# Optimization experiments

Measured on AMD Instinct MI355X. Metric: run time of the kernel, lower is better.

The kernel has to match this reference:

```python
import jax, jax.numpy as jnp
import numpy as np

LMAX = 4
NCOEF = (LMAX + 1) ** 2  # 25 spherical-harmonic coefficients
EXPAND = np.repeat(np.arange(LMAX + 1), [2 * l + 1 for l in range(LMAX + 1)])  # per-l -> per-(l,m)
N, E, C, H, HEADS, ACH, VCH, F, G, DE, AEMB, MAXEL = 10000, 50000, 64, 64, 8, 16, 8, 128, 36, 32, 32, 100


def setup_inputs() -> dict:
    ks = jax.random.split(jax.random.key(0), 24)
    f = lambda i, shape, s=1.0: jax.random.normal(ks[i], shape, jnp.float32) * s
    return dict(
        x=f(0, (N, NCOEF, C)),
        edge_index=jax.random.randint(ks[1], (2, E), 0, N),
        atomic_numbers=jax.random.randint(ks[2], (N,), 0, MAXEL),
        edge_distance=jax.random.uniform(ks[3], (E, DE), jnp.float32),
        wigner=f(4, (E, NCOEF, NCOEF), 0.2),
        src_tab=f(5, (MAXEL, AEMB), 0.02), tgt_tab=f(6, (MAXEL, AEMB), 0.02),
        rad_w1=f(7, (DE + 2 * AEMB, 64), 0.1), rad_b1=jnp.zeros((64,), jnp.float32),
        rad_w2=f(8, (64, 64), 0.1), rad_b2=jnp.zeros((64,), jnp.float32),
        rad_w3=f(9, (64, (LMAX + 1) * 2 * C), 0.05), rad_b3=jnp.ones(((LMAX + 1) * 2 * C,), jnp.float32),
        W1=f(10, (2 * C, H), 0.05), W0_extra=f(11, (2 * C, HEADS * ACH + H), 0.05),
        alpha_dot=f(12, (HEADS, ACH), 0.1),
        to_grid=f(13, (G, NCOEF), 0.2), from_grid=f(14, (NCOEF, G), 0.2),
        proj_out=f(15, (HEADS * VCH, C), 0.1),
        gamma1=jnp.ones((C,), jnp.float32), gamma2=jnp.ones((C,), jnp.float32),
        gl_w=f(16, (C, F), 0.1), gl_b=jnp.zeros((F,), jnp.float32),
        ffn_w1=f(17, (C, F), 0.1), ffn_b1=jnp.zeros((F,), jnp.float32),
        ffn_w2=f(18, (F, C), 0.1), ffn_b2=jnp.zeros((C,), jnp.float32),
    )


def _rmsnorm(x, gamma, eps=1e-6):
    # equivariant norm over the coefficient axis, per node/channel
    rms = jnp.sqrt(jnp.mean(x * x, axis=1, keepdims=True) + eps)  # [N,1,C]
    return x / rms * gamma


def _s2_sep_act(gate, x, to_grid, from_grid):
    # separable S2 activation: scalars = silu(gating scalars); l>0 via grid SiLU
    grid = jnp.einsum('gi,nih->ngh', to_grid, x)
    xg = jnp.einsum('ig,ngh->nih', from_grid, jax.nn.silu(grid))
    return jnp.concatenate([jax.nn.silu(gate)[:, None, :], xg[:, 1:, :]], axis=1)


def reference(x, edge_index, atomic_numbers, edge_distance, wigner, src_tab, tgt_tab,
              rad_w1, rad_b1, rad_w2, rad_b2, rad_w3, rad_b3,
              W1, W0_extra, alpha_dot, to_grid, from_grid, proj_out,
              gamma1, gamma2, gl_w, gl_b, ffn_w1, ffn_b1, ffn_w2, ffn_b2):
    src, dst = edge_index[0], edge_index[1]
    # ---- SO2 equivariant graph attention (gather -> rotate -> conv -> act -> attn -> scatter) ----
    h = _rmsnorm(x, gamma1)
    xe = jnp.concatenate([h[src], h[dst]], axis=-1)          # [E,25,2C] edge gather
    xe = jnp.einsum('eij,ejc->eic', wigner, xe)              # rotate into edge frame
    ef = jnp.concatenate([edge_distance, src_tab[atomic_numbers[src]],
                          tgt_tab[atomic_numbers[dst]]], axis=-1)
    r = jax.nn.silu(ef @ rad_w1 + rad_b1)
    r = jax.nn.silu(r @ rad_w2 + rad_b2)
    r = (r @ rad_w3 + rad_b3).reshape(-1, LMAX + 1, 2 * C)[:, EXPAND, :]  # m-shared radial, [E,25,2C]
    xe = xe * r
    extra = xe[:, 0, :] @ W0_extra                           # extra m=0 channels
    alpha_f = extra[:, :HEADS * ACH].reshape(-1, HEADS, ACH)
    gate = extra[:, HEADS * ACH:]                            # [E,H]
    msg = jnp.einsum('eic,ch->eih', xe, W1)                  # [E,25,H]
    msg = _s2_sep_act(gate, msg, to_grid, from_grid)
    # attention weights: softmax over incoming edges of each destination node
    alpha = jnp.einsum('eha,ha->eh', jax.nn.silu(alpha_f), alpha_dot)
    amax = jax.lax.stop_gradient(jax.ops.segment_max(alpha, dst, num_segments=N))
    a = jnp.exp(alpha - amax[dst])
    a = a / (jax.ops.segment_sum(a, dst, num_segments=N)[dst] + 1e-8)
    msg = (msg.reshape(-1, NCOEF, HEADS, VCH) * a[:, None, :, None]).reshape(-1, NCOEF, HEADS * VCH)
    msg = jnp.einsum('eji,ejc->eic', wigner, msg)            # rotate back (D^T)
    agg = jax.ops.segment_sum(msg, dst, num_segments=N)      # scatter-add, [N,25,H]
    x = x + agg @ proj_out
    # ---- feed-forward with separable S2 activation ----
    h = _rmsnorm(x, gamma2)
    gate = h[:, 0, :] @ gl_w + gl_b
    f1 = jnp.einsum('nic,cf->nif', h, ffn_w1)
    f1 = jnp.concatenate([f1[:, :1, :] + ffn_b1, f1[:, 1:, :]], axis=1)  # bias on l=0 only
    f1 = _s2_sep_act(gate, f1, to_grid, from_grid)
    f2 = jnp.einsum('nif,fc->nic', f1, ffn_w2)
    f2 = jnp.concatenate([f2[:, :1, :] + ffn_b2, f2[:, 1:, :]], axis=1)
    return x + f2
```

## Files before the change

kernel.cpp:

```cpp
#include <hip/hip_runtime.h>
#include <hip/hip_bf16.h>

#define NN 10000
#define NE 50000

typedef __attribute__((ext_vector_type(8))) short bfrag8;
typedef __attribute__((ext_vector_type(4))) short s16x4;
typedef __attribute__((ext_vector_type(4))) float f32x4;

__device__ __forceinline__ float silu_f(float v){ return v / (1.0f + __expf(-v)); }
__device__ __forceinline__ short f2b(float f){
  unsigned u = __float_as_uint(f);
  u += 0x7fffu + ((u>>16)&1u);
  return (short)(u>>16);
}
__device__ __forceinline__ float b2f(short s){
  return __uint_as_float(((unsigned)(unsigned short)s)<<16);
}

__global__ __launch_bounds__(256) void k_rms1(const float* __restrict__ x,
                                              const float* __restrict__ gamma,
                                              __hip_bfloat16* __restrict__ h){
  int idx = blockIdx.x*256 + threadIdx.x;
  if (idx >= NN*64) return;
  int n = idx>>6, c = idx&63;
  const float* xp = x + (size_t)n*1600 + c;
  float ss = 0.f;
#pragma unroll
  for (int i=0;i<25;i++){ float v = xp[i*64]; ss += v*v; }
  float inv = gamma[c] * rsqrtf(ss*(1.f/25.f) + 1e-6f);
  __hip_bfloat16* hp = h + (size_t)n*1600 + c;
#pragma unroll
  for (int i=0;i<25;i++) hp[i*64] = __float2bfloat16(xp[i*64]*inv);
}

__global__ void k_wprep(const float* __restrict__ W1, const float* __restrict__ tog,
                        const float* __restrict__ fromg, const float* __restrict__ proj,
                        const float* __restrict__ fw1, const float* __restrict__ fw2,
                        const float* __restrict__ rw1, const float* __restrict__ rw2,
                        const float* __restrict__ rw3, const float* __restrict__ w0e,
                        short* __restrict__ w1t, short* __restrict__ togA,
                        short* __restrict__ fgA, short* __restrict__ projT,
                        short* __restrict__ fw1T, short* __restrict__ fw2T,
                        short* __restrict__ rw1T, short* __restrict__ rw2T,
                        short* __restrict__ rw3T, short* __restrict__ w0eP){
  int t0 = blockIdx.x*blockDim.x + threadIdx.x;
  int stride = gridDim.x*blockDim.x;
  for (int idx=t0; idx<64*136; idx+=stride){
    int hh = idx/136, k = idx-136*hh;
    w1t[idx] = (k<128) ? f2b(W1[k*64+hh]) : (short)0;
  }
  for (int idx=t0; idx<48*40; idx+=stride){
    int g = idx/40, i = idx-40*g;
    togA[idx] = (g<36 && i<25) ? f2b(tog[g*25+i]) : (short)0;
  }
  for (int idx=t0; idx<32*72; idx+=stride){
    int j = idx/72, g = idx-72*j;
    fgA[idx] = (j<25 && g<36) ? f2b(fromg[j*36+g]) : (short)0;
  }
  for (int idx=t0; idx<64*64; idx+=stride){
    int c = idx>>6, k = idx&63;
    projT[idx] = f2b(proj[k*64+c]);
  }
  for (int idx=t0; idx<128*64; idx+=stride){
    int f = idx>>6, c = idx&63;
    fw1T[idx] = f2b(fw1[c*128+f]);
  }
  for (int idx=t0; idx<64*128; idx+=stride){
    int c = idx>>7, f = idx&127;
    fw2T[idx] = f2b(fw2[f*64+c]);
  }
  for (int idx=t0; idx<64*96; idx+=stride){
    int n = idx/96, k = idx-96*n;
    rw1T[idx] = f2b(rw1[k*64+n]);
  }
  for (int idx=t0; idx<64*64; idx+=stride){
    int n = idx>>6, k = idx&63;
    rw2T[idx] = f2b(rw2[k*64+n]);
  }
  for (int idx=t0; idx<640*64; idx+=stride){
    int n = idx>>6, k = idx&63;
    rw3T[idx] = f2b(rw3[(size_t)k*640+n]);
  }
  for (int idx=t0; idx<128*192; idx+=stride)
    w0eP[idx] = f2b(w0e[idx]);
}

__global__ __launch_bounds__(256,4) void k_radial(
  const int* __restrict__ ei, const int* __restrict__ an,
  const float* __restrict__ edist,
  const float* __restrict__ stab, const float* __restrict__ ttab,
  const short* __restrict__ rw1T, const float* __restrict__ rb1,
  const short* __restrict__ rw2T, const float* __restrict__ rb2,
  const short* __restrict__ rw3T, const float* __restrict__ rb3,
  short* __restrict__ rfS)
{
  __shared__ __align__(16) short SP[7936];
  const int tid = threadIdx.x;
  const int wv = tid>>6, lane = tid&63, lo = lane&15, q = lane>>4;
  const int e0 = blockIdx.x*32;
  {
    int e = tid>>3;
    int ee = min(e0+e, NE-1);
    int srcE = ei[ee], dstE = ei[NE+ee];
    const float* dp = edist + (size_t)ee*32;
    const float* sp = stab + (size_t)an[srcE]*32;
    const float* tp = ttab + (size_t)an[dstE]*32;
    int kb = tid&7;
#pragma unroll
    for (int it=0; it<12; ++it){
      int k = kb + it*8;
      float v = (k<32) ? dp[k] : (k<64 ? sp[k-32] : tp[k-64]);
      SP[e*104+k] = f2b(v);
    }
  }
  __syncthreads();
  {
    f32x4 zf={0.f,0.f,0.f,0.f}; f32x4 acc[2]={zf,zf};
#pragma unroll
    for (int kt=0;kt<3;kt++){
      bfrag8 a = *(const bfrag8*)&rw1T[(wv*16+lo)*96 + kt*32 + q*8];
#pragma unroll
      for (int et=0;et<2;et++){
        bfrag8 b = *(const bfrag8*)&SP[(et*16+lo)*104 + kt*32 + q*8];
        acc[et] = __builtin_amdgcn_mfma_f32_16x16x32_bf16(a,b,acc[et],0,0,0);
      }
    }
    int n1 = wv*16 + q*4;
    const float4 bb = *(const float4*)&rb1[n1];
#pragma unroll
    for (int et=0;et<2;et++){
      s16x4 o;
      o[0]=f2b(silu_f(acc[et][0]+bb.x)); o[1]=f2b(silu_f(acc[et][1]+bb.y));
      o[2]=f2b(silu_f(acc[et][2]+bb.z)); o[3]=f2b(silu_f(acc[et][3]+bb.w));
      *(s16x4*)&SP[3328 + (et*16+lo)*72 + n1] = o;
    }
  }
  __syncthreads();
  {
    f32x4 zf={0.f,0.f,0.f,0.f}; f32x4 acc[2]={zf,zf};
#pragma unroll
    for (int kt=0;kt<2;kt++){
      bfrag8 a = *(const bfrag8*)&rw2T[(wv*16+lo)*64 + kt*32 + q*8];
#pragma unroll
      for (int et=0;et<2;et++){
        bfrag8 b = *(const bfrag8*)&SP[3328 + (et*16+lo)*72 + kt*32 + q*8];
        acc[et] = __builtin_amdgcn_mfma_f32_16x16x32_bf16(a,b,acc[et],0,0,0);
      }
    }
    int n2 = wv*16 + q*4;
    const float4 bb = *(const float4*)&rb2[n2];
#pragma unroll
    for (int et=0;et<2;et++){
      s16x4 o;
      o[0]=f2b(silu_f(acc[et][0]+bb.x)); o[1]=f2b(silu_f(acc[et][1]+bb.y));
      o[2]=f2b(silu_f(acc[et][2]+bb.z)); o[3]=f2b(silu_f(acc[et][3]+bb.w));
      *(s16x4*)&SP[5632 + (et*16+lo)*72 + n2] = o;
    }
  }
  __syncthreads();
  {
    bfrag8 bfr[2][2];
#pragma unroll
    for (int et=0;et<2;et++)
#pragma unroll
      for (int kt=0;kt<2;kt++)
        bfr[et][kt] = *(const bfrag8*)&SP[5632 + (et*16+lo)*72 + kt*32 + q*8];
    for (int mi=0; mi<10; ++mi){
      int n3base = (wv + mi*4)*16;
      f32x4 zf={0.f,0.f,0.f,0.f}; f32x4 acc[2]={zf,zf};
#pragma unroll
      for (int kt=0;kt<2;kt++){
        bfrag8 a = *(const bfrag8*)&rw3T[(size_t)(n3base+lo)*64 + kt*32 + q*8];
        acc[0] = __builtin_amdgcn_mfma_f32_16x16x32_bf16(a,bfr[0][kt],acc[0],0,0,0);
        acc[1] = __builtin_amdgcn_mfma_f32_16x16x32_bf16(a,bfr[1][kt],acc[1],0,0,0);
      }
      int n3 = n3base + q*4;
      const float4 bb = *(const float4*)&rb3[n3];
#pragma unroll
      for (int et=0;et<2;et++){
        int e = e0 + et*16 + lo;
        if (e < NE){
          s16x4 o;
          o[0]=f2b(acc[et][0]+bb.x); o[1]=f2b(acc[et][1]+bb.y);
          o[2]=f2b(acc[et][2]+bb.z); o[3]=f2b(acc[et][3]+bb.w);
          *(s16x4*)&rfS[(size_t)e*640 + n3] = o;
        }
      }
    }
  }
}

__global__ __launch_bounds__(256,4) void k_edge(
  const __hip_bfloat16* __restrict__ h, const int* __restrict__ ei,
  const float* __restrict__ wig,
  const short* __restrict__ w1t, const short* __restrict__ togA,
  const short* __restrict__ fgA, const short* __restrict__ w0eP,
  const float* __restrict__ adot,
  const short* __restrict__ rfS, float* __restrict__ asum,
  float* __restrict__ agg)
{
  __shared__ __align__(16) short POOL[16288];
  float* rfull = (float*)&POOL[14592];
  float* gateL = (float*)&POOL[15872];
  float* ahead = (float*)&POOL[16000];
  float* exL   = (float*)&POOL[16032];
  const int tid = threadIdx.x;
  const int wv = tid>>6, lane = tid&63, lo = lane&15, q = lane>>4;
  const int e = blockIdx.x;
  const int src = ei[e], dst = ei[NE+e];

  {
    int4 z; z.x=0; z.y=0; z.z=0; z.w=0;
    int4* zp = (int4*)POOL;
    for (int idx=tid; idx<960; idx+=256) zp[idx] = z;
  }
  __syncthreads();
  for (int idx=tid; idx<625; idx+=256){
    int i = idx/25, j = idx-25*i;
    short v = f2b(wig[(size_t)e*625+idx]);
    POOL[5120 + i*40 + j] = v;
    POOL[6400 + j*40 + i] = v;
  }
  {
    const __hip_bfloat16* hs = h + (size_t)src*1600;
    const __hip_bfloat16* hd = h + (size_t)dst*1600;
    for (int idx=tid; idx<400; idx+=256){
      int nh = idx/200, rem = idx-200*nh;
      int j = rem>>3, cg = rem&7;
      const __hip_bfloat16* hp = nh ? hd : hs;
      uint4 v = *(const uint4*)(hp + j*64 + cg*8);
      unsigned el[8] = {v.x&0xffffu, v.x>>16, v.y&0xffffu, v.y>>16,
                        v.z&0xffffu, v.z>>16, v.w&0xffffu, v.w>>16};
      int cb = nh*64 + cg*8;
#pragma unroll
      for (int qq=0;qq<8;qq++) POOL[(cb+qq)*40 + j] = (short)el[qq];
    }
  }
  for (int idx=tid; idx<640; idx+=256) rfull[idx] = b2f(rfS[(size_t)e*640+idx]);
  __syncthreads();

  {
    f32x4 zf = {0.f,0.f,0.f,0.f};
    f32x4 acc[2][2] = {{zf,zf},{zf,zf}};
    bfrag8 b0 = *(const bfrag8*)&POOL[5120 + (lo)*40 + q*8];
    bfrag8 b1 = *(const bfrag8*)&POOL[5120 + (16+lo)*40 + q*8];
#pragma unroll
    for (int t=0;t<2;t++){
      int mrow = (2*wv+t)*16 + lo;
      bfrag8 a = *(const bfrag8*)&POOL[mrow*40 + q*8];
      acc[t][0] = __builtin_amdgcn_mfma_f32_16x16x32_bf16(a, b0, acc[t][0], 0,0,0);
      acc[t][1] = __builtin_amdgcn_mfma_f32_16x16x32_bf16(a, b1, acc[t][1], 0,0,0);
    }
#pragma unroll
    for (int t=0;t<2;t++){
      int c0 = (2*wv+t)*16 + q*4;
#pragma unroll
      for (int nt=0;nt<2;nt++){
        int i = nt*16 + lo;
        int l = (i>=16)?4:((i>=9)?3:((i>=4)?2:((i>=1)?1:0)));
        const f32x4 rv = *(const f32x4*)&rfull[l*128 + c0];
        s16x4 o;
#pragma unroll
        for (int r=0;r<4;r++) o[r] = f2b(acc[t][nt][r]*rv[r]);
        *(s16x4*)&POOL[7680 + i*136 + c0] = o;
      }
    }
  }
  __syncthreads();

  {
    if (tid < 96){
      float s0=0.f, s1=0.f;
      for (int c=0; c<128; c+=2){
        unsigned xp = *(const unsigned*)&POOL[7680 + c];
        float x0 = b2f((short)(xp&0xffffu)), x1 = b2f((short)(xp>>16));
        unsigned wp0 = *(const unsigned*)&w0eP[c*192 + 2*tid];
        unsigned wp1 = *(const unsigned*)&w0eP[(c+1)*192 + 2*tid];
        s0 += x0*b2f((short)(wp0&0xffffu)) + x1*b2f((short)(wp1&0xffffu));
        s1 += x0*b2f((short)(wp0>>16))     + x1*b2f((short)(wp1>>16));
      }
      if (tid < 64){
        int n0 = 2*tid;
        exL[n0]   = silu_f(s0)*adot[n0];
        exL[n0+1] = silu_f(s1)*adot[n0+1];
      } else {
        int g0 = 2*tid - 128;
        gateL[g0]   = silu_f(s0);
        gateL[g0+1] = silu_f(s1);
      }
    }
  }
  {
    const int hh = wv*16 + lo;
    f32x4 zf = {0.f,0.f,0.f,0.f};
    f32x4 acc[2] = {zf,zf};
#pragma unroll
    for (int kt=0;kt<4;kt++){
      bfrag8 b = *(const bfrag8*)&w1t[hh*136 + kt*32 + q*8];
#pragma unroll
      for (int t=0;t<2;t++){
        bfrag8 a = *(const bfrag8*)&POOL[7680 + (t*16+lo)*136 + kt*32 + q*8];
        acc[t] = __builtin_amdgcn_mfma_f32_16x16x32_bf16(a, b, acc[t], 0,0,0);
      }
    }
#pragma unroll
    for (int t=0;t<2;t++){
      s16x4 o;
#pragma unroll
      for (int r=0;r<4;r++) o[r] = f2b(acc[t][r]);
      *(s16x4*)&POOL[12032 + hh*40 + t*16 + q*4] = o;
    }
  }
  __syncthreads();

  if (tid < 8){
    float s = 0.f;
#pragma unroll
    for (int a=0;a<16;a++) s += exL[tid*16+a];
    float eh = __expf(s);
    ahead[tid] = eh;
    unsafeAtomicAdd(&asum[(size_t)dst*8 + tid], eh);
  }
  {
    const int hh = wv*16 + lo;
    bfrag8 b = *(const bfrag8*)&POOL[12032 + hh*40 + q*8];
    f32x4 zf = {0.f,0.f,0.f,0.f};
    f32x4 acc[3] = {zf,zf,zf};
#pragma unroll
    for (int t=0;t<3;t++){
      bfrag8 a = *(const bfrag8*)&togA[(t*16+lo)*40 + q*8];
      acc[t] = __builtin_amdgcn_mfma_f32_16x16x32_bf16(a, b, acc[t], 0,0,0);
    }
#pragma unroll
    for (int t=0;t<3;t++){
      s16x4 o;
#pragma unroll
      for (int r=0;r<4;r++) o[r] = f2b(silu_f(acc[t][r]));
      *(s16x4*)&POOL[hh*72 + t*16 + q*4] = o;
    }
  }
  __syncthreads();

  {
    const int hh = wv*16 + lo;
    f32x4 zf = {0.f,0.f,0.f,0.f};
    f32x4 acc[2] = {zf,zf};
#pragma unroll
    for (int kt=0;kt<2;kt++){
      bfrag8 b = *(const bfrag8*)&POOL[hh*72 + kt*32 + q*8];
#pragma unroll
      for (int t=0;t<2;t++){
        bfrag8 a = *(const bfrag8*)&fgA[(t*16+lo)*72 + kt*32 + q*8];
        acc[t] = __builtin_amdgcn_mfma_f32_16x16x32_bf16(a, b, acc[t], 0,0,0);
      }
    }
    float ah = ahead[hh>>3];
#pragma unroll
    for (int t=0;t<2;t++){
      s16x4 o;
#pragma unroll
      for (int r=0;r<4;r++){
        int j = t*16 + q*4 + r;
        float v = acc[t][r];
        if (j==0) v = gateL[hh];
        o[r] = f2b(v*ah);
      }
      *(s16x4*)&POOL[7680 + hh*40 + t*16 + q*4] = o;
    }
  }
  __syncthreads();

  {
    const int hh = wv*16 + lo;
    bfrag8 b = *(const bfrag8*)&POOL[7680 + hh*40 + q*8];
    f32x4 zf = {0.f,0.f,0.f,0.f};
    f32x4 acc[2] = {zf,zf};
#pragma unroll
    for (int t=0;t<2;t++){
      bfrag8 a = *(const bfrag8*)&POOL[6400 + (t*16+lo)*40 + q*8];
      acc[t] = __builtin_amdgcn_mfma_f32_16x16x32_bf16(a, b, acc[t], 0,0,0);
    }
    float* aggp = agg + (size_t)dst*1600;
#pragma unroll
    for (int t=0;t<2;t++){
#pragma unroll
      for (int r=0;r<4;r++){
        int i = t*16 + q*4 + r;
        if (i<25) unsafeAtomicAdd(&aggp[i*64+hh], acc[t][r]);
      }
    }
  }
}

__global__ __launch_bounds__(256,4) void k_node(
  const float* __restrict__ x, const float* __restrict__ aggin,
  const float* __restrict__ asum,
  const short* __restrict__ projT, const float* __restrict__ gamma2,
  const float* __restrict__ glw, const float* __restrict__ glb,
  const short* __restrict__ fw1T, const float* __restrict__ fb1,
  const short* __restrict__ fw2T, const float* __restrict__ fb2,
  const short* __restrict__ togA, const short* __restrict__ fgA,
  float* __restrict__ out)
{
  __shared__ __align__(16) short P[19072];
  float* xF    = (float*)P;
  short* sgB   = P + 4352;
  short* hh2B  = P + 4352;
  short* f1B   = P + 13568;
  short* aggB  = P + 13568;
  short* xgB   = P + 13568;
  float* invc  = ((float*)P) + 9344;
  float* gateF = ((float*)P) + 9408;
  const int tid = threadIdx.x;
  const int wv = tid>>6, lane = tid&63, lo = lane&15, q = lane>>4;
  const int n = blockIdx.x;
  const s16x4 z4 = {0,0,0,0};

  for (int idx=tid; idx<400; idx+=256){
    int i = idx>>4, k = idx&15;
    float sc = 1.f/(asum[(size_t)n*8 + (k>>1)] + 1e-8f);
    const float4 v = *(const float4*)(aggin + (size_t)n*1600 + (size_t)idx*4);
    s16x4 o; o[0]=f2b(v.x*sc); o[1]=f2b(v.y*sc); o[2]=f2b(v.z*sc); o[3]=f2b(v.w*sc);
    *(s16x4*)&aggB[i*72 + k*4] = o;
  }
  for (int idx=tid; idx<126; idx+=256)
    *(s16x4*)&hh2B[25*72 + idx*4] = z4;
  for (int idx=tid; idx<512; idx+=256){
    int f = idx>>2, gg = 48 + (idx&3)*4;
    *(s16x4*)&sgB[f*72 + gg] = z4;
  }
  __syncthreads();

  {
    f32x4 zf={0.f,0.f,0.f,0.f}; f32x4 acc[2]={zf,zf};
    const int c = wv*16 + lo;
#pragma unroll
    for (int kt=0;kt<2;kt++){
      bfrag8 b = *(const bfrag8*)&projT[c*64 + kt*32 + q*8];
#pragma unroll
      for (int t=0;t<2;t++){
        bfrag8 a = *(const bfrag8*)&aggB[(t*16+lo)*72 + kt*32 + q*8];
        acc[t] = __builtin_amdgcn_mfma_f32_16x16x32_bf16(a,b,acc[t],0,0,0);
      }
    }
#pragma unroll
    for (int t=0;t<2;t++)
#pragma unroll
      for (int r=0;r<4;r++){
        int i = t*16 + q*4 + r;
        if (i<25) xF[i*68+c] = acc[t][r] + x[(size_t)n*1600 + i*64 + c];
      }
  }
  __syncthreads();
  if (tid<64){
    float ss=0.f;
#pragma unroll
    for (int i=0;i<25;i++){ float v = xF[i*68+tid]; ss += v*v; }
    invc[tid] = gamma2[tid]*rsqrtf(ss*(1.f/25.f)+1e-6f);
  }
  __syncthreads();
  for (int idx=tid; idx<1600; idx+=256){
    int i=idx>>6, c=idx&63;
    hh2B[i*72+c] = f2b(xF[i*68+c]*invc[c]);
  }
  if (tid<128){
    float a = glb[tid];
#pragma unroll 8
    for (int c=0;c<64;c++) a += xF[c]*invc[c]*glw[c*128+tid];
    gateF[tid] = silu_f(a);
  }
  __syncthreads();

  {
    f32x4 zf={0.f,0.f,0.f,0.f}; f32x4 acc[2][2]={{zf,zf},{zf,zf}};
#pragma unroll
    for (int kt=0;kt<2;kt++){
      bfrag8 a0 = *(const bfrag8*)&hh2B[(lo)*72 + kt*32 + q*8];
      bfrag8 a1 = *(const bfrag8*)&hh2B[(16+lo)*72 + kt*32 + q*8];
#pragma unroll
      for (int s=0;s<2;s++){
        int f = wv*32 + s*16 + lo;
        bfrag8 b = *(const bfrag8*)&fw1T[f*64 + kt*32 + q*8];
        acc[0][s] = __builtin_amdgcn_mfma_f32_16x16x32_bf16(a0,b,acc[0][s],0,0,0);
        acc[1][s] = __builtin_amdgcn_mfma_f32_16x16x32_bf16(a1,b,acc[1][s],0,0,0);
      }
    }
#pragma unroll
    for (int s=0;s<2;s++){
      int f = wv*32 + s*16 + lo;
      float bb = fb1[f];
#pragma unroll
      for (int t=0;t<2;t++){
        s16x4 o;
#pragma unroll
        for (int r=0;r<4;r++){
          int i = t*16+q*4+r;
          o[r] = f2b(acc[t][s][r] + (i==0 ? bb : 0.f));
        }
        *(s16x4*)&f1B[f*40 + t*16 + q*4] = o;
      }
    }
  }
  __syncthreads();

  {
    f32x4 zf={0.f,0.f,0.f,0.f}; f32x4 acc[3][2]={{zf,zf},{zf,zf},{zf,zf}};
    bfrag8 a0 = *(const bfrag8*)&togA[(lo)*40 + q*8];
    bfrag8 a1 = *(const bfrag8*)&togA[(16+lo)*40 + q*8];
    bfrag8 a2 = *(const bfrag8*)&togA[(32+lo)*40 + q*8];
#pragma unroll
    for (int s=0;s<2;s++){
      int f = wv*32 + s*16 + lo;
      bfrag8 b = *(const bfrag8*)&f1B[f*40 + q*8];
      acc[0][s] = __builtin_amdgcn_mfma_f32_16x16x32_bf16(a0,b,acc[0][s],0,0,0);
      acc[1][s] = __builtin_amdgcn_mfma_f32_16x16x32_bf16(a1,b,acc[1][s],0,0,0);
      acc[2][s] = __builtin_amdgcn_mfma_f32_16x16x32_bf16(a2,b,acc[2][s],0,0,0);
    }
#pragma unroll
    for (int s=0;s<2;s++){
      int f = wv*32 + s*16 + lo;
#pragma unroll
      for (int t=0;t<3;t++){
        s16x4 o;
#pragma unroll
        for (int r=0;r<4;r++) o[r] = f2b(silu_f(acc[t][s][r]));
        *(s16x4*)&sgB[f*72 + t*16 + q*4] = o;
      }
    }
  }
  __syncthreads();

  {
    f32x4 zf={0.f,0.f,0.f,0.f}; f32x4 acc[2][2]={{zf,zf},{zf,zf}};
#pragma unroll
    for (int kt=0;kt<2;kt++){
#pragma unroll
      for (int t=0;t<2;t++){
        bfrag8 b = *(const bfrag8*)&fgA[(t*16+lo)*72 + kt*32 + q*8];
#pragma unroll
        for (int s=0;s<2;s++){
          bfrag8 a = *(const bfrag8*)&sgB[(wv*32+s*16+lo)*72 + kt*32 + q*8];
          acc[s][t] = __builtin_amdgcn_mfma_f32_16x16x32_bf16(a,b,acc[s][t],0,0,0);
        }
      }
    }
#pragma unroll
    for (int s=0;s<2;s++){
      int f0 = wv*32 + s*16 + q*4;
#pragma unroll
      for (int t=0;t<2;t++){
        int j = t*16 + lo;
        s16x4 o;
#pragma unroll
        for (int r=0;r<4;r++)
          o[r] = f2b(j==0 ? gateF[f0+r] : acc[s][t][r]);
        *(s16x4*)&xgB[j*136 + f0] = o;
      }
    }
  }
  __syncthreads();

  {
    f32x4 zf={0.f,0.f,0.f,0.f}; f32x4 acc[2]={zf,zf};
    const int c = wv*16 + lo;
#pragma unroll
    for (int kt=0;kt<4;kt++){
      bfrag8 b = *(const bfrag8*)&fw2T[c*128 + kt*32 + q*8];
#pragma unroll
      for (int t=0;t<2;t++){
        bfrag8 a = *(const bfrag8*)&xgB[(t*16+lo)*136 + kt*32 + q*8];
        acc[t] = __builtin_amdgcn_mfma_f32_16x16x32_bf16(a,b,acc[t],0,0,0);
      }
    }
    float bb = fb2[c];
#pragma unroll
    for (int t=0;t<2;t++)
#pragma unroll
      for (int r=0;r<4;r++){
        int i = t*16 + q*4 + r;
        if (i<25)
          out[(size_t)n*1600 + i*64 + c] = xF[i*68+c] + acc[t][r] + (i==0 ? bb : 0.f);
      }
  }
}

extern "C" void kernel_launch(void* const* d_in, const int* in_sizes, int n_in,
                              void* d_out, int out_size, void* d_ws, size_t ws_size,
                              hipStream_t stream) {
  (void)in_sizes; (void)n_in; (void)ws_size;
  const float* x     = (const float*)d_in[0];
  const int*   ei    = (const int*)d_in[1];
  const int*   an    = (const int*)d_in[2];
  const float* edist = (const float*)d_in[3];
  const float* wig   = (const float*)d_in[4];
  const float* stab  = (const float*)d_in[5];
  const float* ttab  = (const float*)d_in[6];
  const float* rw1   = (const float*)d_in[7];
  const float* rb1   = (const float*)d_in[8];
  const float* rw2   = (const float*)d_in[9];
  const float* rb2   = (const float*)d_in[10];
  const float* rw3   = (const float*)d_in[11];
  const float* rb3   = (const float*)d_in[12];
  const float* W1    = (const float*)d_in[13];
  const float* w0e   = (const float*)d_in[14];
  const float* adot  = (const float*)d_in[15];
  const float* tog   = (const float*)d_in[16];
  const float* fromg = (const float*)d_in[17];
  const float* proj  = (const float*)d_in[18];
  const float* g1    = (const float*)d_in[19];
  const float* g2    = (const float*)d_in[20];
  const float* glw   = (const float*)d_in[21];
  const float* glb   = (const float*)d_in[22];
  const float* fw1   = (const float*)d_in[23];
  const float* fb1   = (const float*)d_in[24];
  const float* fw2   = (const float*)d_in[25];
  const float* fb2   = (const float*)d_in[26];
  float* out = (float*)d_out;

  char* wsb = (char*)d_ws;
  __hip_bfloat16* hbuf = (__hip_bfloat16*)(wsb);
  short* rfS   = (short*)(wsb + 32000000);
  float* asum  = (float*)(wsb + 96000000);
  short* w1t   = (short*)(wsb + 96320128);
  short* togA  = (short*)(wsb + 96337600);
  short* fgA   = (short*)(wsb + 96341504);
  short* projT = (short*)(wsb + 96346112);
  short* fw1T  = (short*)(wsb + 96354304);
  short* fw2T  = (short*)(wsb + 96370688);
  short* rw1T  = (short*)(wsb + 96387072);
  short* rw2T  = (short*)(wsb + 96399360);
  short* rw3T  = (short*)(wsb + 96407552);
  short* w0eP  = (short*)(wsb + 96489472);

  hipMemsetAsync(asum, 0, (size_t)NN*8*sizeof(float), stream);
  hipMemsetAsync(d_out, 0, (size_t)out_size*sizeof(float), stream);

  k_wprep<<<32, 256, 0, stream>>>(W1, tog, fromg, proj, fw1, fw2, rw1, rw2, rw3, w0e,
                                  w1t, togA, fgA, projT, fw1T, fw2T,
                                  rw1T, rw2T, rw3T, w0eP);
  k_rms1  <<<(NN*64+255)/256, 256, 0, stream>>>(x, g1, hbuf);
  k_radial<<<(NE+31)/32, 256, 0, stream>>>(ei, an, edist, stab, ttab,
                                           rw1T, rb1, rw2T, rb2, rw3T, rb3, rfS);
  k_edge  <<<NE, 256, 0, stream>>>(hbuf, ei, wig, w1t, togA, fgA, w0eP, adot,
                                   rfS, asum, out);
  k_node  <<<NN, 256, 0, stream>>>(x, out, asum, projT, g2, glw, glb,
                                   fw1T, fb1, fw2T, fb2, togA, fgA, out);
}
```

Measured before the change: 1.115 ms.

## Pre-transpose wigner and node features, async LDS loads, MFMA alpha projection in edge kernel

```diff
diff --git a/kernel.cpp b/kernel.cpp
--- a/kernel.cpp
+++ b/kernel.cpp
@@ -6,6 +6,7 @@
 
 typedef __attribute__((ext_vector_type(8))) short bfrag8;
 typedef __attribute__((ext_vector_type(4))) short s16x4;
+typedef __attribute__((ext_vector_type(8))) short s16x8;
 typedef __attribute__((ext_vector_type(4))) float f32x4;
 
 __device__ __forceinline__ float silu_f(float v){ return v / (1.0f + __expf(-v)); }
@@ -17,21 +18,35 @@
 __device__ __forceinline__ float b2f(short s){
   return __uint_as_float(((unsigned)(unsigned short)s)<<16);
 }
+__device__ __forceinline__ void gload_lds16(const void* g, void* l){
+  __builtin_amdgcn_global_load_lds(
+      (const __attribute__((address_space(1))) void*)g,
+      (__attribute__((address_space(3))) void*)l, 16, 0, 0);
+}
 
 __global__ __launch_bounds__(256) void k_rms1(const float* __restrict__ x,
                                               const float* __restrict__ gamma,
-                                              __hip_bfloat16* __restrict__ h){
+                                              short* __restrict__ hT){
   int idx = blockIdx.x*256 + threadIdx.x;
   if (idx >= NN*64) return;
   int n = idx>>6, c = idx&63;
   const float* xp = x + (size_t)n*1600 + c;
-  float ss = 0.f;
-#pragma unroll
-  for (int i=0;i<25;i++){ float v = xp[i*64]; ss += v*v; }
+  float v[25]; float ss = 0.f;
+#pragma unroll
+  for (int i=0;i<25;i++){ v[i] = xp[i*64]; ss += v[i]*v[i]; }
   float inv = gamma[c] * rsqrtf(ss*(1.f/25.f) + 1e-6f);
-  __hip_bfloat16* hp = h + (size_t)n*1600 + c;
-#pragma unroll
-  for (int i=0;i<25;i++) hp[i*64] = __float2bfloat16(xp[i*64]*inv);
+  short* hp = hT + (size_t)n*2048 + c*32;
+  const int sw = (c>>1)&3;
+#pragma unroll
+  for (int s=0;s<4;s++){
+    s16x8 o;
+#pragma unroll
+    for (int k=0;k<8;k++){
+      int j = s*8 + k;
+      o[k] = (j<25) ? f2b(v[j]*inv) : (short)0;
+    }
+    *(s16x8*)(hp + ((s ^ sw)<<3)) = o;
+  }
 }
 
 __global__ void k_wprep(const float* __restrict__ W1, const float* __restrict__ tog,
@@ -43,7 +58,7 @@
                         short* __restrict__ fgA, short* __restrict__ projT,
                         short* __restrict__ fw1T, short* __restrict__ fw2T,
                         short* __restrict__ rw1T, short* __restrict__ rw2T,
-                        short* __restrict__ rw3T, short* __restrict__ w0eP){
+                        short* __restrict__ rw3T, short* __restrict__ w0eT){
   int t0 = blockIdx.x*blockDim.x + threadIdx.x;
   int stride = gridDim.x*blockDim.x;
   for (int idx=t0; idx<64*136; idx+=stride){
@@ -82,8 +97,25 @@
     int n = idx>>6, k = idx&63;
     rw3T[idx] = f2b(rw3[(size_t)k*640+n]);
   }
-  for (int idx=t0; idx<128*192; idx+=stride)
-    w0eP[idx] = f2b(w0e[idx]);
+  for (int idx=t0; idx<192*128; idx+=stride){
+    int m = idx>>7, c = idx&127;
+    w0eT[idx] = f2b(w0e[c*192+m]);
+  }
+}
+
+__global__ __launch_bounds__(256) void k_wigprep(const float* __restrict__ wig,
+                                                 short* __restrict__ wigP){
+  const int e = blockIdx.x;
+  const float* w = wig + (size_t)e*625;
+  short* o = wigP + (size_t)e*1600;
+  for (int idx=threadIdx.x; idx<1600; idx+=256){
+    int half = (idx >= 800) ? 1 : 0;
+    int rr = idx - half*800;
+    int i = rr>>5, j = rr&31;
+    float v = 0.f;
+    if (j < 25) v = half ? w[j*25+i] : w[i*25+j];
+    o[idx] = f2b(v);
+  }
 }
 
 __global__ __launch_bounds__(256,4) void k_radial(
@@ -191,67 +223,42 @@
   }
 }
 
-__global__ __launch_bounds__(256,4) void k_edge(
-  const __hip_bfloat16* __restrict__ h, const int* __restrict__ ei,
-  const float* __restrict__ wig,
+__global__ __launch_bounds__(256,8) void k_edge(
+  const short* __restrict__ hT, const int* __restrict__ ei,
+  const short* __restrict__ wigP,
   const short* __restrict__ w1t, const short* __restrict__ togA,
-  const short* __restrict__ fgA, const short* __restrict__ w0eP,
+  const short* __restrict__ fgA, const short* __restrict__ w0eT,
   const float* __restrict__ adot,
   const short* __restrict__ rfS, float* __restrict__ asum,
   float* __restrict__ agg)
 {
-  __shared__ __align__(16) short POOL[16288];
-  float* rfull = (float*)&POOL[14592];
-  float* gateL = (float*)&POOL[15872];
-  float* ahead = (float*)&POOL[16000];
-  float* exL   = (float*)&POOL[16032];
+  __shared__ __align__(16) short SH[7312];
+  float* gateL = (float*)&SH[7168];
+  float* ahead = (float*)&SH[7296];
   const int tid = threadIdx.x;
   const int wv = tid>>6, lane = tid&63, lo = lane&15, q = lane>>4;
   const int e = blockIdx.x;
   const int src = ei[e], dst = ei[NE+e];
 
   {
-    int4 z; z.x=0; z.y=0; z.z=0; z.w=0;
-    int4* zp = (int4*)POOL;
-    for (int idx=tid; idx<960; idx+=256) zp[idx] = z;
-  }
-  __syncthreads();
-  for (int idx=tid; idx<625; idx+=256){
-    int i = idx/25, j = idx-25*i;
-    short v = f2b(wig[(size_t)e*625+idx]);
-    POOL[5120 + i*40 + j] = v;
-    POOL[6400 + j*40 + i] = v;
-  }
-  {
-    const __hip_bfloat16* hs = h + (size_t)src*1600;
-    const __hip_bfloat16* hd = h + (size_t)dst*1600;
-    for (int idx=tid; idx<400; idx+=256){
-      int nh = idx/200, rem = idx-200*nh;
-      int j = rem>>3, cg = rem&7;
-      const __hip_bfloat16* hp = nh ? hd : hs;
-      uint4 v = *(const uint4*)(hp + j*64 + cg*8);
-      unsigned el[8] = {v.x&0xffffu, v.x>>16, v.y&0xffffu, v.y>>16,
-                        v.z&0xffffu, v.z>>16, v.w&0xffffu, v.w>>16};
-      int cb = nh*64 + cg*8;
-#pragma unroll
-      for (int qq=0;qq<8;qq++) POOL[(cb+qq)*40 + j] = (short)el[qq];
-    }
-  }
-  for (int idx=tid; idx<640; idx+=256) rfull[idx] = b2f(rfS[(size_t)e*640+idx]);
-  __syncthreads();
-
-  {
-    f32x4 zf = {0.f,0.f,0.f,0.f};
-    f32x4 acc[2][2] = {{zf,zf},{zf,zf}};
-    bfrag8 b0 = *(const bfrag8*)&POOL[5120 + (lo)*40 + q*8];
-    bfrag8 b1 = *(const bfrag8*)&POOL[5120 + (16+lo)*40 + q*8];
-#pragma unroll
-    for (int t=0;t<2;t++){
-      int mrow = (2*wv+t)*16 + lo;
-      bfrag8 a = *(const bfrag8*)&POOL[mrow*40 + q*8];
-      acc[t][0] = __builtin_amdgcn_mfma_f32_16x16x32_bf16(a, b0, acc[t][0], 0,0,0);
-      acc[t][1] = __builtin_amdgcn_mfma_f32_16x16x32_bf16(a, b1, acc[t][1], 0,0,0);
-    }
+    const char* g0 = (const char*)(hT + (size_t)src*2048) + wv*1024 + lane*16;
+    const char* g1 = (const char*)(hT + (size_t)dst*2048) + wv*1024 + lane*16;
+    gload_lds16(g0, (char*)SH + wv*1024);
+    gload_lds16(g1, (char*)SH + 4096 + wv*1024);
+  }
+  {
+    const s16x4 z4 = {0,0,0,0};
+    if (tid < 128) *(s16x4*)&SH[4096 + tid*4] = z4;
+  }
+  const short* wA = wigP + (size_t)e*1600;
+  const short* wT = wA + 800;
+  const bfrag8 wz = {0,0,0,0,0,0,0,0};
+  const bfrag8 wb0 = *(const bfrag8*)&wA[lo*32 + q*8];
+  bfrag8 wb1 = wz;
+  if (lo < 9) wb1 = *(const bfrag8*)&wA[(16+lo)*32 + q*8];
+  s16x4 rvp[2][2];
+  {
+    const short* rrow = rfS + (size_t)e*640;
 #pragma unroll
     for (int t=0;t<2;t++){
       int c0 = (2*wv+t)*16 + q*4;
@@ -259,48 +266,82 @@
       for (int nt=0;nt<2;nt++){
         int i = nt*16 + lo;
         int l = (i>=16)?4:((i>=9)?3:((i>=4)?2:((i>=1)?1:0)));
-        const f32x4 rv = *(const f32x4*)&rfull[l*128 + c0];
-        s16x4 o;
-#pragma unroll
-        for (int r=0;r<4;r++) o[r] = f2b(acc[t][nt][r]*rv[r]);
-        *(s16x4*)&POOL[7680 + i*136 + c0] = o;
-      }
-    }
-  }
-  __syncthreads();
-
-  {
-    if (tid < 96){
-      float s0=0.f, s1=0.f;
-      for (int c=0; c<128; c+=2){
-        unsigned xp = *(const unsigned*)&POOL[7680 + c];
-        float x0 = b2f((short)(xp&0xffffu)), x1 = b2f((short)(xp>>16));
-        unsigned wp0 = *(const unsigned*)&w0eP[c*192 + 2*tid];
-        unsigned wp1 = *(const unsigned*)&w0eP[(c+1)*192 + 2*tid];
-        s0 += x0*b2f((short)(wp0&0xffffu)) + x1*b2f((short)(wp1&0xffffu));
-        s1 += x0*b2f((short)(wp0>>16))     + x1*b2f((short)(wp1>>16));
-      }
-      if (tid < 64){
-        int n0 = 2*tid;
-        exL[n0]   = silu_f(s0)*adot[n0];
-        exL[n0+1] = silu_f(s1)*adot[n0+1];
-      } else {
-        int g0 = 2*tid - 128;
-        gateL[g0]   = silu_f(s0);
-        gateL[g0+1] = silu_f(s1);
+        rvp[t][nt] = *(const s16x4*)&rrow[l*128 + c0];
+      }
+    }
+  }
+  asm volatile("s_waitcnt vmcnt(0)" ::: "memory");
+  __syncthreads();
+
+  f32x4 xacc[2][2];
+  {
+    const f32x4 zf = {0.f,0.f,0.f,0.f};
+#pragma unroll
+    for (int t=0;t<2;t++){
+      int c = (2*wv+t)*16 + lo;
+      bfrag8 a = *(const bfrag8*)&SH[c*32 + ((q ^ ((c>>1)&3))<<3)];
+      xacc[t][0] = __builtin_amdgcn_mfma_f32_16x16x32_bf16(a, wb0, zf, 0,0,0);
+      xacc[t][1] = __builtin_amdgcn_mfma_f32_16x16x32_bf16(a, wb1, zf, 0,0,0);
+    }
+  }
+  __syncthreads();
+#pragma unroll
+  for (int t=0;t<2;t++){
+    int c0 = (2*wv+t)*16 + q*4;
+#pragma unroll
+    for (int nt=0;nt<2;nt++){
+      int i = nt*16 + lo;
+      s16x4 rv = rvp[t][nt];
+      s16x4 o;
+#pragma unroll
+      for (int r=0;r<4;r++) o[r] = f2b(xacc[t][nt][r]*b2f(rv[r]));
+      *(s16x4*)&SH[i*136 + c0] = o;
+    }
+  }
+  __syncthreads();
+
+  {
+    bfrag8 xb[4];
+#pragma unroll
+    for (int kt=0;kt<4;kt++) xb[kt] = *(const bfrag8*)&SH[kt*32 + q*8];
+    const f32x4 zf = {0.f,0.f,0.f,0.f};
+#pragma unroll
+    for (int t=0;t<3;t++){
+      const int mt = wv*3 + t;
+      f32x4 acc = zf;
+#pragma unroll
+      for (int kt=0;kt<4;kt++){
+        bfrag8 a = *(const bfrag8*)&w0eT[(mt*16+lo)*128 + kt*32 + q*8];
+        acc = __builtin_amdgcn_mfma_f32_16x16x32_bf16(a, xb[kt], acc, 0,0,0);
+      }
+      if (mt < 8){
+        float s = 0.f;
+#pragma unroll
+        for (int r=0;r<4;r++) s += silu_f(acc[r]) * adot[mt*16 + q*4 + r];
+        s += __shfl_xor(s, 16);
+        s += __shfl_xor(s, 32);
+        float eh = __expf(s);
+        if (lane==0){
+          ahead[mt] = eh;
+          unsafeAtomicAdd(&asum[(size_t)dst*8 + mt], eh);
+        }
+      } else if (lo==0){
+        int g0 = mt*16 - 128 + q*4;
+#pragma unroll
+        for (int r=0;r<4;r++) gateL[g0+r] = silu_f(acc[r]);
       }
     }
   }
   {
     const int hh = wv*16 + lo;
-    f32x4 zf = {0.f,0.f,0.f,0.f};
+    const f32x4 zf = {0.f,0.f,0.f,0.f};
     f32x4 acc[2] = {zf,zf};
 #pragma unroll
     for (int kt=0;kt<4;kt++){
       bfrag8 b = *(const bfrag8*)&w1t[hh*136 + kt*32 + q*8];
 #pragma unroll
       for (int t=0;t<2;t++){
-        bfrag8 a = *(const bfrag8*)&POOL[7680 + (t*16+lo)*136 + kt*32 + q*8];
+        bfrag8 a = *(const bfrag8*)&SH[(t*16+lo)*136 + kt*32 + q*8];
         acc[t] = __builtin_amdgcn_mfma_f32_16x16x32_bf16(a, b, acc[t], 0,0,0);
       }
     }
@@ -309,23 +350,15 @@
       s16x4 o;
 #pragma unroll
       for (int r=0;r<4;r++) o[r] = f2b(acc[t][r]);
-      *(s16x4*)&POOL[12032 + hh*40 + t*16 + q*4] = o;
-    }
-  }
-  __syncthreads();
-
-  if (tid < 8){
-    float s = 0.f;
-#pragma unroll
-    for (int a=0;a<16;a++) s += exL[tid*16+a];
-    float eh = __expf(s);
-    ahead[tid] = eh;
-    unsafeAtomicAdd(&asum[(size_t)dst*8 + tid], eh);
-  }
+      *(s16x4*)&SH[4608 + hh*40 + t*16 + q*4] = o;
+    }
+  }
+  __syncthreads();
+
   {
     const int hh = wv*16 + lo;
-    bfrag8 b = *(const bfrag8*)&POOL[12032 + hh*40 + q*8];
-    f32x4 zf = {0.f,0.f,0.f,0.f};
+    bfrag8 b = *(const bfrag8*)&SH[4608 + hh*40 + q*8];
+    const f32x4 zf = {0.f,0.f,0.f,0.f};
     f32x4 acc[3] = {zf,zf,zf};
 #pragma unroll
     for (int t=0;t<3;t++){
@@ -337,18 +370,16 @@
       s16x4 o;
 #pragma unroll
       for (int r=0;r<4;r++) o[r] = f2b(silu_f(acc[t][r]));
-      *(s16x4*)&POOL[hh*72 + t*16 + q*4] = o;
-    }
-  }
-  __syncthreads();
-
+      *(s16x4*)&SH[hh*72 + t*16 + q*4] = o;
+    }
+  }
   {
     const int hh = wv*16 + lo;
-    f32x4 zf = {0.f,0.f,0.f,0.f};
+    const f32x4 zf = {0.f,0.f,0.f,0.f};
     f32x4 acc[2] = {zf,zf};
 #pragma unroll
     for (int kt=0;kt<2;kt++){
-      bfrag8 b = *(const bfrag8*)&POOL[hh*72 + kt*32 + q*8];
+      bfrag8 b = *(const bfrag8*)&SH[hh*72 + kt*32 + q*8];
 #pragma unroll
       for (int t=0;t<2;t++){
         bfrag8 a = *(const bfrag8*)&fgA[(t*16+lo)*72 + kt*32 + q*8];
@@ -362,34 +393,31 @@
 #pragma unroll
       for (int r=0;r<4;r++){
         int j = t*16 + q*4 + r;
-        float v = acc[t][r];
-        if (j==0) v = gateL[hh];
+        float v = (j==0) ? gateL[hh] : acc[t][r];
         o[r] = f2b(v*ah);
       }
-      *(s16x4*)&POOL[7680 + hh*40 + t*16 + q*4] = o;
-    }
-  }
-  __syncthreads();
-
+      *(s16x4*)&SH[4608 + hh*40 + t*16 + q*4] = o;
+    }
+  }
   {
     const int hh = wv*16 + lo;
-    bfrag8 b = *(const bfrag8*)&POOL[7680 + hh*40 + q*8];
-    f32x4 zf = {0.f,0.f,0.f,0.f};
+    bfrag8 b = *(const bfrag8*)&SH[4608 + hh*40 + q*8];
+    const f32x4 zf = {0.f,0.f,0.f,0.f};
     f32x4 acc[2] = {zf,zf};
 #pragma unroll
     for (int t=0;t<2;t++){
-      bfrag8 a = *(const bfrag8*)&POOL[6400 + (t*16+lo)*40 + q*8];
+      bfrag8 a = wz;
+      if (t==0 || lo < 9) a = *(const bfrag8*)&wT[(t*16+lo)*32 + q*8];
       acc[t] = __builtin_amdgcn_mfma_f32_16x16x32_bf16(a, b, acc[t], 0,0,0);
     }
     float* aggp = agg + (size_t)dst*1600;
 #pragma unroll
-    for (int t=0;t<2;t++){
+    for (int t=0;t<2;t++)
 #pragma unroll
       for (int r=0;r<4;r++){
         int i = t*16 + q*4 + r;
         if (i<25) unsafeAtomicAdd(&aggp[i*64+hh], acc[t][r]);
       }
-    }
   }
 }
 
@@ -619,30 +647,32 @@
   float* out = (float*)d_out;
 
   char* wsb = (char*)d_ws;
-  __hip_bfloat16* hbuf = (__hip_bfloat16*)(wsb);
-  short* rfS   = (short*)(wsb + 32000000);
-  float* asum  = (float*)(wsb + 96000000);
-  short* w1t   = (short*)(wsb + 96320128);
-  short* togA  = (short*)(wsb + 96337600);
-  short* fgA   = (short*)(wsb + 96341504);
-  short* projT = (short*)(wsb + 96346112);
-  short* fw1T  = (short*)(wsb + 96354304);
-  short* fw2T  = (short*)(wsb + 96370688);
-  short* rw1T  = (short*)(wsb + 96387072);
-  short* rw2T  = (short*)(wsb + 96399360);
-  short* rw3T  = (short*)(wsb + 96407552);
-  short* w0eP  = (short*)(wsb + 96489472);
+  short* hT    = (short*)(wsb);
+  short* wigP  = (short*)(wsb + 40960000);
+  short* rfS   = (short*)(wsb + 200964096);
+  float* asum  = (float*)(wsb + 264964096);
+  short* w1t   = (short*)(wsb + 265284096);
+  short* togA  = (short*)(wsb + 265301504);
+  short* fgA   = (short*)(wsb + 265305344);
+  short* projT = (short*)(wsb + 265309952);
+  short* fw1T  = (short*)(wsb + 265318144);
+  short* fw2T  = (short*)(wsb + 265334528);
+  short* rw1T  = (short*)(wsb + 265350912);
+  short* rw2T  = (short*)(wsb + 265363200);
+  short* rw3T  = (short*)(wsb + 265371392);
+  short* w0eT  = (short*)(wsb + 265453312);
 
   hipMemsetAsync(asum, 0, (size_t)NN*8*sizeof(float), stream);
   hipMemsetAsync(d_out, 0, (size_t)out_size*sizeof(float), stream);
 
   k_wprep<<<32, 256, 0, stream>>>(W1, tog, fromg, proj, fw1, fw2, rw1, rw2, rw3, w0e,
                                   w1t, togA, fgA, projT, fw1T, fw2T,
-                                  rw1T, rw2T, rw3T, w0eP);
-  k_rms1  <<<(NN*64+255)/256, 256, 0, stream>>>(x, g1, hbuf);
+                                  rw1T, rw2T, rw3T, w0eT);
+  k_wigprep<<<NE, 256, 0, stream>>>(wig, wigP);
+  k_rms1  <<<(NN*64+255)/256, 256, 0, stream>>>(x, g1, hT);
   k_radial<<<(NE+31)/32, 256, 0, stream>>>(ei, an, edist, stab, ttab,
                                            rw1T, rb1, rw2T, rb2, rw3T, rb3, rfS);
-  k_edge  <<<NE, 256, 0, stream>>>(hbuf, ei, wig, w1t, togA, fgA, w0eP, adot,
+  k_edge  <<<NE, 256, 0, stream>>>(hT, ei, wigP, w1t, togA, fgA, w0eT, adot,
                                    rfS, asum, out);
   k_node  <<<NN, 256, 0, stream>>>(x, out, asum, projT, g2, glw, glb,
                                    fw1T, fb1, fw2T, fb2, togA, fgA, out);
```

Result: no change. 1.104 ms (-1.0%).
